# Performance work log

Measured on AMD Instinct MI355X. Metric: run time of the kernel, lower is better.

Reference implementation:

```python
import jax, jax.numpy as jnp
import numpy as np

# ---- static HashEncoder config (matches __init__ defaults) ----
D = 3            # input_dim
L = 16           # num_levels
C = 2            # level_dim
BASE = 16.0      # base_resolution (isotropic)
SCALE = 2.0      # per_level_scale (isotropic)
MAX_PARAMS = 2 ** 19  # log2_hashmap_size = 19

_base = np.full(D, BASE, dtype=np.float64)
_pls = np.full(D, SCALE, dtype=np.float64)
_offsets = [0]
_res = []
_off = 0
for i in range(L):
    r = np.ceil(_base * _pls ** i)
    _res.append(r.astype(np.int64))
    _off += int(min(MAX_PARAMS, np.prod(r)))
    _offsets.append(_off)
TOTAL_PARAMS = _off  # 7,114,752

# spatial-hash primes (instant-ngp convention; prime for dim 0 is 1)
PRIMES = np.array([1, 2654435761, 805459861], dtype=np.uint32)
# corner bit patterns for the 2^D = 8 cube corners, shape [8, D]
BITS = np.array([[(c >> d) & 1 for d in range(D)] for c in range(2 ** D)], dtype=np.uint32)
BITS_MASK = BITS.astype(bool)


def _encode_level(x01, embeddings, l):
    """x01: [B, D] normalized coords in [0, 1]; returns [B, C]."""
    scale = (_base * _pls ** l - 1.0).astype(np.float32)        # per-dim grid scale
    res = _res[l]                                               # per-dim resolution
    level_size = _offsets[l + 1] - _offsets[l]
    pos = x01 * scale + 0.5                                     # [B, D]
    pos_grid = jnp.floor(pos)
    frac = pos - pos_grid                                       # [B, D] in [0,1)
    pg = pos_grid.astype(jnp.uint32)                            # [B, D]
    corners = pg[:, None, :] + BITS[None]                       # [B, 8, D]
    # trilinear weights: prod over dims of frac (bit=1) or 1-frac (bit=0)
    w = jnp.prod(jnp.where(BITS_MASK[None], frac[:, None, :], 1.0 - frac[:, None, :]), axis=-1)  # [B, 8]
    if int(np.prod(res)) > level_size:
        # hashed level: xor of per-dim (coord * prime), mod table size
        h = corners * PRIMES[None, None, :]
        idx = (h[..., 0] ^ h[..., 1] ^ h[..., 2]) % jnp.uint32(level_size)
    else:
        # dense level: row-major stride indexing
        stride = np.array([1, res[0], res[0] * res[1]], dtype=np.uint32)
        idx = jnp.sum(corners * stride[None, None, :], axis=-1)  # [B, 8]
    g = embeddings[_offsets[l] + idx.astype(jnp.int32)]          # [B, 8, C] gather
    return jnp.sum(w[..., None] * g, axis=1)                     # [B, C]


def setup_inputs() -> dict:
    key = jax.random.key(0)
    k1, k2 = jax.random.split(key)
    B = 1048576
    inputs = jax.random.uniform(k1, (B, D), dtype=jnp.float32, minval=-1.0, maxval=1.0)
    # reset_parameters(): uniform(-0.1, 0.1)
    embeddings = jax.random.uniform(k2, (TOTAL_PARAMS, C), dtype=jnp.float32, minval=-0.1, maxval=0.1)
    return {"inputs": inputs, "embeddings": embeddings}


def reference(inputs, embeddings):
    # forward(inputs, size=1): normalize [-1,1] -> [0,1]
    x01 = (inputs + 1.0) * 0.5
    outs = [_encode_level(x01, embeddings, l) for l in range(L)]
    return jnp.concatenate(outs, axis=-1)  # [B, L*C] = [B, 32]
```

## Files before the change

kernel.cpp:

```cpp
#include <hip/hip_runtime.h>


static constexpr uint32_t P1 = 2654435761u;
static constexpr uint32_t P2 = 805459861u;
static constexpr uint32_t NPARAMS = 7114752u;
static constexpr uint32_t HMASK = 524287u;

__device__ inline uint32_t bf16_bits(float f) {
    uint32_t u = __float_as_uint(f);
    return (u + 0x7FFFu + ((u >> 16) & 1u)) >> 16;
}

__global__ __launch_bounds__(256) void convert_bf16(
    const float* __restrict__ emb, uint32_t* __restrict__ tab)
{
    const uint32_t i = blockIdx.x * 256u + threadIdx.x;
    const float4 v = ((const float4*)emb)[i];
    uint2 o;
    o.x = bf16_bits(v.x) | (bf16_bits(v.y) << 16);
    o.y = bf16_bits(v.z) | (bf16_bits(v.w) << 16);
    ((uint2*)tab)[i] = o;
}

__global__ __launch_bounds__(256) void enc_level2(
    const float* __restrict__ inp,
    const uint32_t* __restrict__ tab,
    float2* __restrict__ stage,
    int npoints)
{
    const uint32_t l = blockIdx.y;
    const uint32_t pair = blockIdx.x * 256u + threadIdx.x;

    const float2* in2 = (const float2*)inp;
    const float2 ab = in2[3u * pair + 0u];
    const float2 cd = in2[3u * pair + 1u];
    const float2 ef = in2[3u * pair + 2u];

    const uint32_t res = 16u << l;
    const float scale = (float)(res - 1u);

    uint32_t off;
    if (l >= 3u)      off = 299008u + (l - 3u) * 524288u;
    else if (l == 2u) off = 36864u;
    else if (l == 1u) off = 4096u;
    else              off = 0u;
    const bool hashed = (l >= 3u);
    const uint32_t s = 4u + (hashed ? 0u : l);

    const float xs[2] = {ab.x, cd.y};
    const float ys[2] = {ab.y, ef.x};
    const float zs[2] = {cd.x, ef.y};

    float wx0[2], wx1[2], wyq[2][2], wzq[2][2];
    uint32_t idxA[2][4];
    bool gx_odd[2];
    uint32_t gxq[2];

#pragma unroll
    for (int q = 0; q < 2; ++q) {
        const float x01 = (xs[q] + 1.0f) * 0.5f;
        const float y01 = (ys[q] + 1.0f) * 0.5f;
        const float z01 = (zs[q] + 1.0f) * 0.5f;
        const float posx = x01 * scale + 0.5f;
        const float posy = y01 * scale + 0.5f;
        const float posz = z01 * scale + 0.5f;
        const float fgx = floorf(posx), fgy = floorf(posy), fgz = floorf(posz);
        const float fx = posx - fgx, fy = posy - fgy, fz = posz - fgz;
        const uint32_t gx = (uint32_t)fgx, gy = (uint32_t)fgy, gz = (uint32_t)fgz;

        wx0[q] = 1.0f - fx; wx1[q] = fx;
        wyq[q][0] = 1.0f - fy; wyq[q][1] = fy;
        wzq[q][0] = 1.0f - fz; wzq[q][1] = fz;
        gxq[q] = gx;
        gx_odd[q] = (gx & 1u) != 0u;

        uint32_t yzc[4];
        if (hashed) {
            const uint32_t hy0 = gy * P1, hy1 = hy0 + P1;
            const uint32_t hz0 = gz * P2, hz1 = hz0 + P2;
            yzc[0] = hy0 ^ hz0; yzc[1] = hy1 ^ hz0;
            yzc[2] = hy0 ^ hz1; yzc[3] = hy1 ^ hz1;
        } else {
            const uint32_t dy0 = gy << s, dy1 = dy0 + (1u << s);
            const uint32_t dz0 = gz << (2u * s), dz1 = dz0 + (1u << (2u * s));
            yzc[0] = dy0 + dz0; yzc[1] = dy1 + dz0;
            yzc[2] = dy0 + dz1; yzc[3] = dy1 + dz1;
        }
#pragma unroll
        for (int c = 0; c < 4; ++c)
            idxA[q][c] = hashed ? ((gxq[q] ^ yzc[c]) & HMASK)
                                : (gxq[q] + yzc[c]);
    }

    uint2 pr[2][4];
#pragma unroll
    for (int q = 0; q < 2; ++q)
#pragma unroll
        for (int c = 0; c < 4; ++c)
            pr[q][c] = *(const uint2*)(tab + off + (idxA[q][c] & ~1u));

    uint32_t vBo[2][4];
#pragma unroll
    for (int q = 0; q < 2; ++q) {
        if (gx_odd[q]) {
#pragma unroll
            for (int c = 0; c < 4; ++c) {
                const uint32_t idxB = hashed
                    ? (((gxq[q] + 1u) ^ (idxA[q][c] ^ gxq[q])) & HMASK)
                    : (idxA[q][c] + 1u);
                vBo[q][c] = tab[off + idxB];
            }
        }
    }

    float4 r;
    float* rp = (float*)&r;
#pragma unroll
    for (int q = 0; q < 2; ++q) {
        float sx = 0.0f, sy = 0.0f;
#pragma unroll
        for (int c = 0; c < 4; ++c) {
            const uint32_t lo = idxA[q][c] & 1u;
            const uint32_t vA = lo ? pr[q][c].y : pr[q][c].x;
            const uint32_t vBe = lo ? pr[q][c].x : pr[q][c].y;
            const uint32_t vB = gx_odd[q] ? vBo[q][c] : vBe;
            const float wyz = wyq[q][c & 1] * wzq[q][c >> 1];
            const float eAx = __uint_as_float(vA << 16);
            const float eAy = __uint_as_float(vA & 0xFFFF0000u);
            const float eBx = __uint_as_float(vB << 16);
            const float eBy = __uint_as_float(vB & 0xFFFF0000u);
            sx = fmaf(wyz, fmaf(wx0[q], eAx, wx1[q] * eBx), sx);
            sy = fmaf(wyz, fmaf(wx0[q], eAy, wx1[q] * eBy), sy);
        }
        rp[2 * q + 0] = sx;
        rp[2 * q + 1] = sy;
    }

    ((float4*)stage)[(size_t)l * ((uint32_t)npoints >> 1) + pair] = r;
}

__global__ __launch_bounds__(256) void transpose_out(
    const float2* __restrict__ stage, float4* __restrict__ out4, int npoints)
{
    __shared__ float2 t[256][17];
    const uint32_t p0 = blockIdx.x * 256u;
    const uint32_t tid = threadIdx.x;

#pragma unroll
    for (int l = 0; l < 16; ++l)
        t[tid][l] = stage[(size_t)l * (uint32_t)npoints + p0 + tid];
    __syncthreads();

#pragma unroll
    for (int k = 0; k < 8; ++k) {
        const uint32_t f = (uint32_t)k * 256u + tid;
        const uint32_t p = f >> 3, c = f & 7u;
        const float2 a = t[p][2u * c];
        const float2 b = t[p][2u * c + 1u];
        out4[(size_t)(p0 + p) * 8u + c] = make_float4(a.x, a.y, b.x, b.y);
    }
}

__global__ __launch_bounds__(256) void hashenc_fwd(
    const float* __restrict__ inp, const float* __restrict__ emb,
    float* __restrict__ out, int npoints)
{
    const uint32_t tid = blockIdx.x * 256u + threadIdx.x;
    const uint32_t p = tid >> 4, l = tid & 15u;
    if (p >= (uint32_t)npoints) return;
    const float x01 = (inp[p * 3u + 0u] + 1.0f) * 0.5f;
    const float y01 = (inp[p * 3u + 1u] + 1.0f) * 0.5f;
    const float z01 = (inp[p * 3u + 2u] + 1.0f) * 0.5f;
    const uint32_t res = 16u << l;
    const float scale = (float)(res - 1u);
    const float posx = x01 * scale + 0.5f, posy = y01 * scale + 0.5f, posz = z01 * scale + 0.5f;
    const float fgx = floorf(posx), fgy = floorf(posy), fgz = floorf(posz);
    const float fx = posx - fgx, fy = posy - fgy, fz = posz - fgz;
    const uint32_t gx = (uint32_t)fgx, gy = (uint32_t)fgy, gz = (uint32_t)fgz;
    uint32_t off;
    if (l >= 3u)      off = 299008u + (l - 3u) * 524288u;
    else if (l == 2u) off = 36864u;
    else if (l == 1u) off = 4096u;
    else              off = 0u;
    const bool hashed = (l >= 3u);
    const uint32_t s = 4u + (hashed ? 0u : l);
    const float wx[2] = {1.0f - fx, fx}, wy[2] = {1.0f - fy, fy}, wz[2] = {1.0f - fz, fz};
    float2 g[8]; float w[8];
#pragma unroll
    for (int c = 0; c < 8; ++c) {
        const uint32_t bx = (uint32_t)c & 1u, by = ((uint32_t)c >> 1) & 1u, bz = ((uint32_t)c >> 2) & 1u;
        const uint32_t cx = gx + bx, cy = gy + by, cz = gz + bz;
        const uint32_t hidx = (cx ^ (cy * P1) ^ (cz * P2)) & HMASK;
        const uint32_t didx = cx + (cy << s) + (cz << (2u * s));
        const uint32_t idx  = hashed ? hidx : didx;
        w[c] = wx[bx] * wy[by] * wz[bz];
        g[c] = *(const float2*)(emb + 2u * (off + idx));
    }
    float sx = 0.0f, sy = 0.0f;
#pragma unroll
    for (int c = 0; c < 8; ++c) { sx = fmaf(w[c], g[c].x, sx); sy = fmaf(w[c], g[c].y, sy); }
    *(float2*)(out + (size_t)p * 32u + (size_t)l * 2u) = make_float2(sx, sy);
}

extern "C" void kernel_launch(void* const* d_in, const int* in_sizes, int n_in,
                              void* d_out, int out_size, void* d_ws, size_t ws_size,
                              hipStream_t stream) {
    const float* inp = (const float*)d_in[0];
    const float* emb = (const float*)d_in[1];
    float* out = (float*)d_out;
    const int npoints = in_sizes[0] / 3;

    const size_t tab_bytes = (size_t)NPARAMS * 4u;
    const size_t stage_bytes = (size_t)npoints * 16u * 8u;
    const size_t need = tab_bytes + stage_bytes;

    if (ws_size >= need && (npoints & 511) == 0) {
        uint32_t* tab = (uint32_t*)d_ws;
        float2* stage = (float2*)((char*)d_ws + tab_bytes);

        const int conv_units = (int)(NPARAMS * 2u / 4u);
        convert_bf16<<<(conv_units + 255) / 256, 256, 0, stream>>>(emb, tab);

        dim3 g1(npoints / 512, 16);
        enc_level2<<<g1, 256, 0, stream>>>(inp, tab, stage, npoints);

        transpose_out<<<npoints / 256, 256, 0, stream>>>(stage, (float4*)out, npoints);
    } else {
        const int total = npoints * 16;
        hashenc_fwd<<<(total + 255) / 256, 256, 0, stream>>>(inp, emb, out, npoints);
    }
}
```

Baseline: 590.7 us.

## Pre-pack input coordinates and use nontemporal loads/stores for staging and output

Adds a pack_input kernel that rearranges each point pair's coordinates into a float4 plus float2 buffer, so each of the 16 per-level blocks reads them with two aligned vector loads instead of three float2 loads. The staging writes, the staging reads in the transpose and the final output stores now use nontemporal hints, which keep streaming data from displacing the bf16 embedding table in cache. This costs an extra kernel launch plus workspace and traffic for the packed copy, and the packed path only runs when the workspace is large enough.

```diff
diff --git a/kernel.cpp b/kernel.cpp
--- a/kernel.cpp
+++ b/kernel.cpp
@@ -5,6 +5,9 @@
 static constexpr uint32_t P2 = 805459861u;
 static constexpr uint32_t NPARAMS = 7114752u;
 static constexpr uint32_t HMASK = 524287u;
+
+typedef float f32x4 __attribute__((ext_vector_type(4)));
+typedef float f32x2 __attribute__((ext_vector_type(2)));
 
 __device__ inline uint32_t bf16_bits(float f) {
     uint32_t u = __float_as_uint(f);
@@ -22,19 +25,47 @@
     ((uint2*)tab)[i] = o;
 }
 
+__global__ __launch_bounds__(256) void pack_input(
+    const float* __restrict__ inp, float4* __restrict__ pA,
+    float2* __restrict__ pB, int npairs)
+{
+    const uint32_t u = blockIdx.x * 256u + threadIdx.x;
+    if (u >= (uint32_t)npairs) return;
+    const float2* in2 = (const float2*)inp;
+    const float2 ab = in2[3u * u + 0u];
+    const float2 cd = in2[3u * u + 1u];
+    const float2 ef = in2[3u * u + 2u];
+    const f32x4 a = {ab.x, ab.y, cd.y, ef.x};
+    const f32x2 b = {cd.x, ef.y};
+    __builtin_nontemporal_store(a, (f32x4*)&pA[u]);
+    __builtin_nontemporal_store(b, (f32x2*)&pB[u]);
+}
+
 __global__ __launch_bounds__(256) void enc_level2(
+    const float4* __restrict__ pA,
+    const float2* __restrict__ pB,
     const float* __restrict__ inp,
     const uint32_t* __restrict__ tab,
     float2* __restrict__ stage,
     int npoints)
 {
     const uint32_t l = blockIdx.y;
-    const uint32_t pair = blockIdx.x * 256u + threadIdx.x;
-
-    const float2* in2 = (const float2*)inp;
-    const float2 ab = in2[3u * pair + 0u];
-    const float2 cd = in2[3u * pair + 1u];
-    const float2 ef = in2[3u * pair + 2u];
+    const uint32_t u = blockIdx.x * 256u + threadIdx.x;
+
+    float xs[2], ys[2], zs[2];
+    if (pA) {
+        const float4 a = pA[u];
+        const float2 b = pB[u];
+        xs[0] = a.x; ys[0] = a.y; zs[0] = b.x;
+        xs[1] = a.z; ys[1] = a.w; zs[1] = b.y;
+    } else {
+        const float2* in2 = (const float2*)inp;
+        const float2 ab = in2[3u * u + 0u];
+        const float2 cd = in2[3u * u + 1u];
+        const float2 ef = in2[3u * u + 2u];
+        xs[0] = ab.x; ys[0] = ab.y; zs[0] = cd.x;
+        xs[1] = cd.y; ys[1] = ef.x; zs[1] = ef.y;
+    }
 
     const uint32_t res = 16u << l;
     const float scale = (float)(res - 1u);
@@ -46,10 +77,6 @@
     else              off = 0u;
     const bool hashed = (l >= 3u);
     const uint32_t s = 4u + (hashed ? 0u : l);
-
-    const float xs[2] = {ab.x, cd.y};
-    const float ys[2] = {ab.y, ef.x};
-    const float zs[2] = {cd.x, ef.y};
 
     float wx0[2], wx1[2], wyq[2][2], wzq[2][2];
     uint32_t idxA[2][4];
@@ -113,17 +140,16 @@
         }
     }
 
-    float4 r;
-    float* rp = (float*)&r;
+    f32x4 r;
 #pragma unroll
     for (int q = 0; q < 2; ++q) {
         float sx = 0.0f, sy = 0.0f;
 #pragma unroll
         for (int c = 0; c < 4; ++c) {
             const uint32_t lo = idxA[q][c] & 1u;
-            const uint32_t vA = lo ? pr[q][c].y : pr[q][c].x;
+            const uint32_t vA  = lo ? pr[q][c].y : pr[q][c].x;
             const uint32_t vBe = lo ? pr[q][c].x : pr[q][c].y;
-            const uint32_t vB = gx_odd[q] ? vBo[q][c] : vBe;
+            const uint32_t vB  = gx_odd[q] ? vBo[q][c] : vBe;
             const float wyz = wyq[q][c & 1] * wzq[q][c >> 1];
             const float eAx = __uint_as_float(vA << 16);
             const float eAy = __uint_as_float(vA & 0xFFFF0000u);
@@ -132,11 +158,12 @@
             sx = fmaf(wyz, fmaf(wx0[q], eAx, wx1[q] * eBx), sx);
             sy = fmaf(wyz, fmaf(wx0[q], eAy, wx1[q] * eBy), sy);
         }
-        rp[2 * q + 0] = sx;
-        rp[2 * q + 1] = sy;
-    }
-
-    ((float4*)stage)[(size_t)l * ((uint32_t)npoints >> 1) + pair] = r;
+        r[2 * q + 0] = sx;
+        r[2 * q + 1] = sy;
+    }
+
+    __builtin_nontemporal_store(r,
+        (f32x4*)&((float4*)stage)[(size_t)l * ((uint32_t)npoints >> 1) + u]);
 }
 
 __global__ __launch_bounds__(256) void transpose_out(
@@ -147,8 +174,11 @@
     const uint32_t tid = threadIdx.x;
 
 #pragma unroll
-    for (int l = 0; l < 16; ++l)
-        t[tid][l] = stage[(size_t)l * (uint32_t)npoints + p0 + tid];
+    for (int l = 0; l < 16; ++l) {
+        const f32x2 v = __builtin_nontemporal_load(
+            (const f32x2*)&stage[(size_t)l * (uint32_t)npoints + p0 + tid]);
+        t[tid][l] = make_float2(v.x, v.y);
+    }
     __syncthreads();
 
 #pragma unroll
@@ -157,7 +187,9 @@
         const uint32_t p = f >> 3, c = f & 7u;
         const float2 a = t[p][2u * c];
         const float2 b = t[p][2u * c + 1u];
-        out4[(size_t)(p0 + p) * 8u + c] = make_float4(a.x, a.y, b.x, b.y);
+        const f32x4 v = {a.x, a.y, b.x, b.y};
+        __builtin_nontemporal_store(v,
+            (f32x4*)&out4[(size_t)(p0 + p) * 8u + c]);
     }
 }
 
@@ -209,20 +241,32 @@
     const float* emb = (const float*)d_in[1];
     float* out = (float*)d_out;
     const int npoints = in_sizes[0] / 3;
-
-    const size_t tab_bytes = (size_t)NPARAMS * 4u;
+    const int npairs = npoints / 2;
+
+    const size_t tab_bytes   = (size_t)NPARAMS * 4u;
     const size_t stage_bytes = (size_t)npoints * 16u * 8u;
-    const size_t need = tab_bytes + stage_bytes;
-
-    if (ws_size >= need && (npoints & 511) == 0) {
-        uint32_t* tab = (uint32_t*)d_ws;
-        float2* stage = (float2*)((char*)d_ws + tab_bytes);
+    const size_t pA_bytes    = (size_t)npairs * 16u;
+    const size_t pB_bytes    = (size_t)npairs * 8u;
+    const size_t need_base   = tab_bytes + stage_bytes;
+    const size_t need_pack   = need_base + pA_bytes + pB_bytes;
+
+    if (ws_size >= need_base && (npoints & 511) == 0) {
+        uint32_t* tab  = (uint32_t*)d_ws;
+        float2* stage  = (float2*)((char*)d_ws + tab_bytes);
+        float4* pA = nullptr;
+        float2* pB = nullptr;
 
         const int conv_units = (int)(NPARAMS * 2u / 4u);
         convert_bf16<<<(conv_units + 255) / 256, 256, 0, stream>>>(emb, tab);
 
+        if (ws_size >= need_pack) {
+            pA = (float4*)((char*)d_ws + need_base);
+            pB = (float2*)((char*)d_ws + need_base + pA_bytes);
+            pack_input<<<(npairs + 255) / 256, 256, 0, stream>>>(inp, pA, pB, npairs);
+        }
+
         dim3 g1(npoints / 512, 16);
-        enc_level2<<<g1, 256, 0, stream>>>(inp, tab, stage, npoints);
+        enc_level2<<<g1, 256, 0, stream>>>(pA, pB, inp, tab, stage, npoints);
 
         transpose_out<<<npoints / 256, 256, 0, stream>>>(stage, (float4*)out, npoints);
     } else {
```

New measurement: 597.8 us. About the same (+1.2%).
